# Kernel optimization log

Measured on AMD Instinct MI355X. Metric: run time of the kernel, lower is better.

Reference implementation:

```python
import jax, jax.numpy as jnp
import numpy as np

H = 48; W = 48; C_IN = 32; C_OUT = 64
L = 4                      # liftsamples
RADIUS = 3                 # neighborhood radius
CMCO = 16                  # LieConv PointConv fixed mid channels
FOCAL = W / np.pi          # equidistant fisheye focal
CX, CY = (W - 1) / 2.0, (H - 1) / 2.0
EPS = 1e-7


def _build_neighbor_indices(h, w, radius):
    offs = [(dx, dy) for dy in range(-radius, radius + 1)
            for dx in range(-radius, radius + 1)
            if dx * dx + dy * dy <= radius * radius]
    offs = np.array(offs, dtype=np.int64)  # (k,2) as (dx,dy)
    yy, xx = np.meshgrid(np.arange(h), np.arange(w), indexing='ij')
    yy = yy.reshape(-1, 1); xx = xx.reshape(-1, 1)
    ny = yy + offs[None, :, 1]; nx = xx + offs[None, :, 0]
    valid = (ny >= 0) & (ny < h) & (nx >= 0) & (nx < w)
    idx = ny * w + nx
    return np.where(valid, idx, -1).astype(np.int32)  # (h*w, k)


def swish(x):
    return x * jax.nn.sigmoid(x)


def so3_exp(wvec):
    # Rodrigues: (...,3) -> (...,3,3)
    th = jnp.maximum(jnp.linalg.norm(wvec, axis=-1, keepdims=True), EPS)
    k = wvec / th
    kx, ky, kz = k[..., 0], k[..., 1], k[..., 2]
    z = jnp.zeros_like(kx)
    K = jnp.stack([jnp.stack([z, -kz, ky], -1),
                   jnp.stack([kz, z, -kx], -1),
                   jnp.stack([-ky, kx, z], -1)], -2)
    th = th[..., None]
    I = jnp.eye(3, dtype=wvec.dtype)
    return I + jnp.sin(th) * K + (1.0 - jnp.cos(th)) * (K @ K)


def so3_log(R):
    # (...,3,3) -> (...,3)
    tr = R[..., 0, 0] + R[..., 1, 1] + R[..., 2, 2]
    cos = jnp.clip((tr - 1.0) * 0.5, -1.0 + 1e-6, 1.0 - 1e-6)
    th = jnp.arccos(cos)
    v = jnp.stack([R[..., 2, 1] - R[..., 1, 2],
                   R[..., 0, 2] - R[..., 2, 0],
                   R[..., 1, 0] - R[..., 0, 1]], -1)
    return v * (th / (2.0 * jnp.sin(th)))[..., None]


def setup_inputs() -> dict:
    key = jax.random.key(0)
    ks = jax.random.split(key, 6)
    def lin(k, fi, fo):
        return jax.random.normal(k, (fi, fo), jnp.float32) / np.sqrt(fi)
    return {
        'x': jax.random.normal(ks[0], (2, C_IN, H, W), jnp.float32),
        'neighbor_idx': jnp.asarray(_build_neighbor_indices(H, W, RADIUS)),
        'W1': lin(ks[1], 3, 32), 'b1': jnp.zeros((32,), jnp.float32),
        'W2': lin(ks[2], 32, 32), 'b2': jnp.zeros((32,), jnp.float32),
        'W3': lin(ks[3], 32, CMCO), 'b3': jnp.zeros((CMCO,), jnp.float32),
        'Wl': lin(ks[4], CMCO * C_IN, C_OUT), 'bl': jnp.zeros((C_OUT,), jnp.float32),
    }


def _lift_log(dtype):
    # pixel grid -> unit rays -> so(3) log of lifted group elems, shape (n*L, 3)
    u = jnp.arange(W, dtype=dtype); v = jnp.arange(H, dtype=dtype)
    uu, vv = jnp.meshgrid(u, v)               # 'xy' indexing, (H,W)
    dx = (uu - CX).reshape(-1); dy = (vv - CY).reshape(-1)
    r = jnp.sqrt(dx * dx + dy * dy)
    theta = r / FOCAL
    rs = jnp.maximum(r, EPS)
    rays = jnp.stack([jnp.sin(theta) * dx / rs,
                      jnp.sin(theta) * dy / rs,
                      jnp.cos(theta)], -1)    # (n,3)
    pz = jnp.clip(rays[:, 2], -1.0 + 1e-6, 1.0 - 1e-6)
    ang = jnp.arccos(pz)
    axis = jnp.stack([-rays[:, 1], rays[:, 0], jnp.zeros_like(pz)], -1)
    axis = axis / jnp.maximum(jnp.linalg.norm(axis, axis=-1, keepdims=True), EPS)
    Rp = so3_exp(axis * ang[:, None])          # (n,3,3), Rp @ e3 = ray
    alphas = jnp.arange(L, dtype=dtype) * (2.0 * np.pi / L)
    Rz = so3_exp(jnp.stack([jnp.zeros_like(alphas), jnp.zeros_like(alphas), alphas], -1))
    Rlift = jnp.einsum('nij,ljk->nlik', Rp, Rz)  # (n,L,3,3)
    return so3_log(Rlift).reshape(H * W * L, 3)


def reference(x, neighbor_idx, W1, b1, W2, b2, W3, b3, Wl, bl):
    bs, c, h, w = x.shape
    n = h * w
    k = neighbor_idx.shape[1]
    nL, K = n * L, k * L

    a = _lift_log(x.dtype)                                   # (nL,3)

    valid = neighbor_idx >= 0                                # (n,k)
    safe_pix = jnp.maximum(neighbor_idx, 0).astype(jnp.int32)
    # lifted neighbor indices: query lift copy l sees all (j, l') neighbors
    nb_lift = safe_pix[:, None, :, None] * L + jnp.arange(L, dtype=jnp.int32)[None, None, None, :]
    nb_lift = jnp.broadcast_to(nb_lift, (n, L, k, L)).reshape(nL, K)
    nb_pix = jnp.broadcast_to(safe_pix[:, None, :, None], (n, L, k, L)).reshape(nL, K)
    mask = jnp.broadcast_to(valid[:, None, :, None], (n, L, k, L)).reshape(nL, K)

    # pairwise group elements: log(exp(-b) @ exp(a))
    b_log = a[nb_lift]                                       # (nL,K,3)
    Rab = jnp.einsum('qmij,qjk->qmik', so3_exp(-b_log), so3_exp(a))
    ab = so3_log(Rab)                                        # (nL,K,3)

    # kernel MLP (WeightNet: 3 -> 32 -> 32 -> 16, swish)
    hdn = swish(ab @ W1 + b1)
    hdn = swish(hdn @ W2 + b2)
    wts = swish(hdn @ W3 + b3)                               # (nL,K,16)
    wts = jnp.where(mask[..., None], wts, 0.0)

    values = x.transpose(0, 2, 3, 1).reshape(bs, n, c)       # (bs,n,c)
    nv = values[:, nb_pix]                                   # (bs,nL,K,c)
    partial = jnp.einsum('bqmc,qmf->bqcf', nv, wts).reshape(bs, nL, c * CMCO)
    out = partial @ Wl + bl                                  # (bs,nL,c_out)
    out = out.reshape(bs, n, L, -1).mean(axis=2)             # pool over lift samples
    return out.reshape(bs, h, w, -1).transpose(0, 3, 1, 2)   # (bs,c_out,h,w)
```

## Files before the change

### kernel.cpp

```cpp
#include <hip/hip_runtime.h>

#define WW   48
#define NPIX 2304
#define CIN  32
#define COUT 64
#define KNB  29
#define FCO  16
#define NPJ  (NPIX * KNB)
#define GEN_WAVES  ((NPJ + 6) / 7)
#define GEN_BLOCKS ((GEN_WAVES + 3) / 4)
#define EDGE_BLOCKS ((NPIX * 6 + 1 + 255) / 256)

#define WS_RP64 0
#define WS_EG   165888
#define WS_M0   1050624
#define WS_V    1050688
#define WS_PART 4257856

__device__ __forceinline__ float swish_f(float x) {
    return x * __builtin_amdgcn_rcpf(1.0f + __expf(-x));
}

__device__ __forceinline__ void so3_exp_d(double wx, double wy, double wz, double R[9]) {
    double n  = sqrt(wx * wx + wy * wy + wz * wz);
    double th = fmax(n, 1e-7);
    double kx = wx / th, ky = wy / th, kz = wz / th;
    double s = sin(th), c = cos(th);
    double omc = 1.0 - c;
    R[0] = 1.0 + omc * (kx * kx - 1.0);
    R[1] = -s * kz + omc * kx * ky;
    R[2] =  s * ky + omc * kx * kz;
    R[3] =  s * kz + omc * kx * ky;
    R[4] = 1.0 + omc * (ky * ky - 1.0);
    R[5] = -s * kx + omc * ky * kz;
    R[6] = -s * ky + omc * kz * kx;
    R[7] =  s * kx + omc * kz * ky;
    R[8] = 1.0 + omc * (kz * kz - 1.0);
}

__device__ __forceinline__ void compute_Rp_d(int p, double R[9]) {
    int ui = p % WW, vi = p / WW;
    double dx = (double)ui - 23.5;
    double dy = (double)vi - 23.5;
    double r  = sqrt(dx * dx + dy * dy);
    const double FOCAL = 48.0 / 3.14159265358979323846;
    double theta = r / FOCAL;
    double rs = fmax(r, 1e-7);
    double st = sin(theta);
    double rayx = st * dx / rs;
    double rayy = st * dy / rs;
    double rayz = cos(theta);
    double pz  = fmin(fmax(rayz, -1.0 + 1e-6), 1.0 - 1e-6);
    double ang = acos(pz);
    double ax = -rayy, ay = rayx;
    double an = fmax(sqrt(ax * ax + ay * ay), 1e-7);
    ax /= an; ay /= an;
    so3_exp_d(ax * ang, ay * ang, 0.0, R);
}

__device__ __forceinline__ void mlp_half(float ab0, float ab1, float ab2, const int Q0,
    const float* __restrict__ W1, const float* __restrict__ b1,
    const float* __restrict__ W2, const float* __restrict__ b2,
    const float* __restrict__ W3, const float* __restrict__ b3,
    float* acc3) {
    float accq[16];
    #pragma unroll
    for (int q = 0; q < 16; ++q) accq[q] = b2[Q0 + q];
    #pragma unroll
    for (int i = 0; i < 32; ++i) {
        float h = swish_f(b1[i] + ab0 * W1[i] + ab1 * W1[32 + i] + ab2 * W1[64 + i]);
        #pragma unroll
        for (int q = 0; q < 16; ++q) accq[q] += h * W2[i * 32 + Q0 + q];
    }
    #pragma unroll
    for (int q = 0; q < 16; ++q) {
        float h2 = swish_f(accq[q]);
        #pragma unroll
        for (int f = 0; f < FCO; ++f) acc3[f] += h2 * W3[(Q0 + q) * FCO + f];
    }
}

__device__ __forceinline__ void mlp_eval(float ab0, float ab1, float ab2,
    const float* __restrict__ W1, const float* __restrict__ b1,
    const float* __restrict__ W2, const float* __restrict__ b2,
    const float* __restrict__ W3, const float* __restrict__ b3,
    float* o) {
    float acc3[FCO];
    #pragma unroll
    for (int f = 0; f < FCO; ++f) acc3[f] = b3[f];
    mlp_half(ab0, ab1, ab2, 0,  W1, b1, W2, b2, W3, b3, acc3);
    __builtin_amdgcn_sched_barrier(0);
    mlp_half(ab0, ab1, ab2, 16, W1, b1, W2, b2, W3, b3, acc3);
    #pragma unroll
    for (int f = 0; f < FCO; ++f) o[f] = swish_f(acc3[f]);
}

__global__ __launch_bounds__(256)
void rp_kernel(double* __restrict__ rp64) {
    int p = blockIdx.x * 256 + threadIdx.x;
    if (p >= NPIX) return;
    double R[9];
    compute_Rp_d(p, R);
    #pragma unroll
    for (int e = 0; e < 9; ++e) rp64[p * 9 + e] = R[e];
}

__global__ __launch_bounds__(256)
void vlog2_kernel(const int* __restrict__ nbr, const double* __restrict__ rp64,
                  float* __restrict__ vws) {
    int tid = blockIdx.x * 256 + threadIdx.x;
    if (tid >= NPJ * 4) return;
    int g2 = tid >> 2;
    int d  = tid & 3;
    int p = g2 / KNB, j = g2 - p * KNB;
    int pj = max(nbr[p * KNB + j], 0);
    double Rq[9];
    #pragma unroll
    for (int q = 0; q < 9; ++q) Rq[q] = rp64[p * 9 + q];
    double X[9];
    #pragma unroll
    for (int q = 0; q < 9; ++q) X[q] = 0.0;
    #pragma unroll
    for (int k = 0; k < 3; ++k) {
        double rn0 = rp64[pj * 9 + k * 3 + 0];
        double rn1 = rp64[pj * 9 + k * 3 + 1];
        double rn2 = rp64[pj * 9 + k * 3 + 2];
        #pragma unroll
        for (int jj = 0; jj < 3; ++jj) {
            X[0 * 3 + jj] += rn0 * Rq[k * 3 + jj];
            X[1 * 3 + jj] += rn1 * Rq[k * 3 + jj];
            X[2 * 3 + jj] += rn2 * Rq[k * 3 + jj];
        }
    }
    double c = (d == 0) ? 1.0 : ((d == 2) ? -1.0 : 0.0);
    double s = (d == 1) ? 1.0 : ((d == 3) ? -1.0 : 0.0);
    double M0 =  X[0] * c + X[1] * s;
    double M1 = -X[0] * s + X[1] * c;
    double M2 =  X[2];
    double M3 =  X[3] * c + X[4] * s;
    double M4 = -X[3] * s + X[4] * c;
    double M5 =  X[5];
    double M6 =  X[6] * c + X[7] * s;
    double M7 = -X[6] * s + X[7] * c;
    double M8 =  X[8];
    double tr   = M0 + M4 + M8;
    double cosv = fmin(fmax((tr - 1.0) * 0.5, -1.0 + 1e-6), 1.0 - 1e-6);
    double th   = acos(cosv);
    double svv  = sqrt((1.0 - cosv) * (1.0 + cosv));
    double fac  = th / (2.0 * svv);
    float* dst = vws + g2 * 12 + d * 3;
    dst[0] = (float)((M7 - M5) * fac);
    dst[1] = (float)((M2 - M6) * fac);
    dst[2] = (float)((M3 - M1) * fac);
}

__global__ __launch_bounds__(256)
void mlp1_kernel(const int* __restrict__ nbr,
                 const float* __restrict__ W1, const float* __restrict__ b1,
                 const float* __restrict__ W2, const float* __restrict__ b2,
                 const float* __restrict__ W3, const float* __restrict__ b3,
                 const double* __restrict__ rp64, const float* __restrict__ vws,
                 float* __restrict__ eg, float* __restrict__ m0v,
                 float* __restrict__ part) {
    if (blockIdx.x < GEN_BLOCKS) {
        int wave = blockIdx.x * 4 + (threadIdx.x >> 6);
        int lane = threadIdx.x & 63;
        int slot = lane / 9;
        int e    = lane - slot * 9;
        int g2   = wave * 7 + slot;
        int g2c  = min(g2, NPJ - 1);
        int l1m = e / 3, l2m = e - l1m * 3;
        int l1 = l1m + (l1m >> 1);
        int l2 = l2m + (l2m >> 1);
        int d  = (l1 - l2) & 3;
        const float* vp = vws + g2c * 12 + d * 3;
        float v0 = vp[0], v1 = vp[1], v2 = vp[2];
        float ab0 = (l2m == 0) ? v0 : ((l2m == 1) ?  v1 : -v1);
        float ab1 = (l2m == 0) ? v1 : ((l2m == 1) ? -v0 :  v0);
        float o[FCO];
        mlp_eval(ab0, ab1, v2, W1, b1, W2, b2, W3, b3, o);
        #pragma unroll
        for (int f = 0; f < FCO; ++f) {
            float a = o[f];
            a += __shfl(a, min(lane + 1, 63)) + __shfl(a, min(lane + 2, 63));
            a += __shfl(a, min(lane + 3, 63)) + __shfl(a, min(lane + 6, 63));
            o[f] = a;
        }
        if (e == 0 && lane < 63 && g2 < NPJ) {
            float* dst = part + g2 * FCO;
            #pragma unroll
            for (int f = 0; f < FCO; ++f) dst[f] = o[f];
        }
    } else {
        int g = (blockIdx.x - GEN_BLOCKS) * 256 + threadIdx.x;
        if (g > NPIX * 6) return;
        if (g == NPIX * 6) {
            float o[FCO];
            mlp_eval(0.f, 0.f, 0.f, W1, b1, W2, b2, W3, b3, o);
            #pragma unroll
            for (int f = 0; f < FCO; ++f) m0v[f] = o[f];
            return;
        }
        int pix = g / 6, which = g - pix * 6;
        double R[9];
        #pragma unroll
        for (int q = 0; q < 9; ++q) R[q] = rp64[pix * 9 + q];
        int m = (which < 3) ? which : (which - 3);
        int l = m + (m >> 1);
        double c = (l == 0) ? 1.0 : 0.0;
        double s = (l == 1) ? 1.0 : ((l == 3) ? -1.0 : 0.0);
        double M[9];
        #pragma unroll
        for (int i = 0; i < 3; ++i) {
            M[i * 3 + 0] =  R[i * 3 + 0] * c + R[i * 3 + 1] * s;
            M[i * 3 + 1] = -R[i * 3 + 0] * s + R[i * 3 + 1] * c;
            M[i * 3 + 2] =  R[i * 3 + 2];
        }
        double tr   = M[0] + M[4] + M[8];
        double cosv = fmin(fmax((tr - 1.0) * 0.5, -1.0 + 1e-6), 1.0 - 1e-6);
        double th   = acos(cosv);
        double sv   = sqrt((1.0 - cosv) * (1.0 + cosv));
        double fac  = th / (2.0 * sv);
        float sg = (which < 3) ? 1.f : -1.f;
        float o[FCO];
        mlp_eval(sg * (float)((M[7] - M[5]) * fac),
                 sg * (float)((M[2] - M[6]) * fac),
                 sg * (float)((M[3] - M[1]) * fac),
                 W1, b1, W2, b2, W3, b3, o);
        #pragma unroll
        for (int f = 0; f < FCO; ++f) eg[g * FCO + f] = o[f];
    }
}

__global__ __launch_bounds__(256)
void agg_kernel(const float* __restrict__ x, const int* __restrict__ nbr,
                const float* __restrict__ Wl, const float* __restrict__ bl,
                const float* __restrict__ eg, const float* __restrict__ m0v,
                const float* __restrict__ part, float* __restrict__ out) {
    __shared__ int   spj[KNB];
    __shared__ int   sval[KNB];
    __shared__ float sE[FCO];
    __shared__ float sS[KNB][FCO];
    __shared__ float sxv[2][CIN][KNB];
    __shared__ float sT[2][CIN][FCO];
    __shared__ float spp[256];

    const int p = blockIdx.x;
    const int t = threadIdx.x;

    if (t < KNB) {
        int idx = nbr[p * KNB + t];
        spj[t]  = max(idx, 0);
        sval[t] = (idx >= 0) ? 1 : 0;
    } else if (t >= 32 && t < 32 + FCO) {
        int f = t - 32;
        sE[f] = eg[(p * 6 + 0) * FCO + f] + eg[(p * 6 + 1) * FCO + f]
              + eg[(p * 6 + 2) * FCO + f] + m0v[f];
    }
    __syncthreads();

    for (int e = t; e < 2 * CIN * KNB; e += 256) {
        int bb = e / (CIN * KNB);
        int r  = e - bb * (CIN * KNB);
        int c  = r / KNB;
        int j  = r - c * KNB;
        sxv[bb][c][j] = x[bb * (CIN * NPIX) + c * NPIX + spj[j]];
    }
    for (int idx = t; idx < KNB * FCO; idx += 256) {
        int j = idx >> 4, f = idx & 15;
        float acc = part[(p * KNB + j) * FCO + f];
        int n6 = spj[j] * 6;
        acc += eg[(n6 + 3) * FCO + f] + eg[(n6 + 4) * FCO + f] + eg[(n6 + 5) * FCO + f];
        acc += sE[f];
        sS[j][f] = sval[j] ? acc * 0.25f : 0.f;
    }
    __syncthreads();

    for (int tt = t; tt < 2 * CIN * FCO; tt += 256) {
        int bb = tt >> 9;
        int c  = (tt >> 4) & 31;
        int f  = tt & 15;
        float acc = 0.f;
        #pragma unroll
        for (int j = 0; j < KNB; ++j)
            acc += sxv[bb][c][j] * sS[j][f];
        sT[bb][c][f] = acc;
    }
    __syncthreads();

    {
        int half = t >> 7, q = t & 127, bb = q >> 6, co = q & 63;
        const float* Tb = &sT[bb][0][0];
        float acc = 0.f;
        int cf0 = half * 256;
        #pragma unroll 8
        for (int cf = cf0; cf < cf0 + 256; ++cf)
            acc += Tb[cf] * Wl[cf * COUT + co];
        spp[t] = acc;
    }
    __syncthreads();
    if (t < 128) {
        int bb = t >> 6, co = t & 63;
        out[bb * (COUT * NPIX) + co * NPIX + p] = spp[t] + spp[t + 128] + bl[co];
    }
}

extern "C" void kernel_launch(void* const* d_in, const int* in_sizes, int n_in,
                              void* d_out, int out_size, void* d_ws, size_t ws_size,
                              hipStream_t stream) {
    const float* x  = (const float*)d_in[0];
    const int* nbr  = (const int*)d_in[1];
    const float* W1 = (const float*)d_in[2];
    const float* b1 = (const float*)d_in[3];
    const float* W2 = (const float*)d_in[4];
    const float* b2 = (const float*)d_in[5];
    const float* W3 = (const float*)d_in[6];
    const float* b3 = (const float*)d_in[7];
    const float* Wl = (const float*)d_in[8];
    const float* bl = (const float*)d_in[9];
    float* out = (float*)d_out;

    char* ws = (char*)d_ws;
    double* rp64 = (double*)(ws + WS_RP64);
    float*  eg   = (float*)(ws + WS_EG);
    float*  m0v  = (float*)(ws + WS_M0);
    float*  vws  = (float*)(ws + WS_V);
    float*  part = (float*)(ws + WS_PART);

    hipLaunchKernelGGL(rp_kernel, dim3((NPIX + 255) / 256), dim3(256), 0, stream,
                       rp64);
    hipLaunchKernelGGL(vlog2_kernel, dim3((NPJ * 4 + 255) / 256), dim3(256), 0, stream,
                       nbr, rp64, vws);
    hipLaunchKernelGGL(mlp1_kernel, dim3(GEN_BLOCKS + EDGE_BLOCKS), dim3(256), 0, stream,
                       nbr, W1, b1, W2, b2, W3, b3, rp64, vws, eg, m0v, part);
    hipLaunchKernelGGL(agg_kernel, dim3(NPIX), dim3(256), 0, stream,
                       x, nbr, Wl, bl, eg, m0v, part, out);
}
```

Baseline: 86.80 us.

## Move per-pixel edge MLP into rotation kernel and share Wl loads across batches

The per-pixel edge MLP evaluations (6 per pixel plus the zero-argument one) move out of the mlp1 kernel into the first kernel, which now runs 7 threads per pixel. Each thread recomputes the pixel rotation instead of reading it back from workspace. The mlp1 kernel now handles only the pairwise neighbor MLP. Separately, the final Wl projection in agg_kernel uses 128 threads that each serve both batch items from one Wl load, instead of 256 threads each loading Wl for one batch item. This halves Wl traffic but leaves half the block idle during that phase.

```diff
diff --git a/kernel.cpp b/kernel.cpp
--- a/kernel.cpp
+++ b/kernel.cpp
@@ -9,7 +9,6 @@
 #define NPJ  (NPIX * KNB)
 #define GEN_WAVES  ((NPJ + 6) / 7)
 #define GEN_BLOCKS ((GEN_WAVES + 3) / 4)
-#define EDGE_BLOCKS ((NPIX * 6 + 1 + 255) / 256)
 
 #define WS_RP64 0
 #define WS_EG   165888
@@ -96,13 +95,51 @@
 }
 
 __global__ __launch_bounds__(256)
-void rp_kernel(double* __restrict__ rp64) {
-    int p = blockIdx.x * 256 + threadIdx.x;
-    if (p >= NPIX) return;
+void rpe_kernel(const float* __restrict__ W1, const float* __restrict__ b1,
+                const float* __restrict__ W2, const float* __restrict__ b2,
+                const float* __restrict__ W3, const float* __restrict__ b3,
+                double* __restrict__ rp64, float* __restrict__ eg,
+                float* __restrict__ m0v) {
+    int tid = blockIdx.x * 256 + threadIdx.x;
+    if (tid >= NPIX * 7) return;
+    int p = tid / 7, which = tid - p * 7;
     double R[9];
     compute_Rp_d(p, R);
-    #pragma unroll
-    for (int e = 0; e < 9; ++e) rp64[p * 9 + e] = R[e];
+    if (which == 0) {
+        #pragma unroll
+        for (int e = 0; e < 9; ++e) rp64[p * 9 + e] = R[e];
+    }
+    int w = (which == 0) ? 0 : (which - 1);
+    int m = (w < 3) ? w : (w - 3);
+    float sg = (which == 0) ? 0.f : ((w < 3) ? 1.f : -1.f);
+    int l = m + (m >> 1);
+    double c = (l == 0) ? 1.0 : 0.0;
+    double s = (l == 1) ? 1.0 : ((l == 3) ? -1.0 : 0.0);
+    double M[9];
+    #pragma unroll
+    for (int i = 0; i < 3; ++i) {
+        M[i * 3 + 0] =  R[i * 3 + 0] * c + R[i * 3 + 1] * s;
+        M[i * 3 + 1] = -R[i * 3 + 0] * s + R[i * 3 + 1] * c;
+        M[i * 3 + 2] =  R[i * 3 + 2];
+    }
+    double tr   = M[0] + M[4] + M[8];
+    double cosv = fmin(fmax((tr - 1.0) * 0.5, -1.0 + 1e-6), 1.0 - 1e-6);
+    double th   = acos(cosv);
+    double sv   = sqrt((1.0 - cosv) * (1.0 + cosv));
+    double fac  = th / (2.0 * sv);
+    float o[FCO];
+    mlp_eval(sg * (float)((M[7] - M[5]) * fac),
+             sg * (float)((M[2] - M[6]) * fac),
+             sg * (float)((M[3] - M[1]) * fac),
+             W1, b1, W2, b2, W3, b3, o);
+    if (which > 0) {
+        float* dst = eg + (p * 6 + w) * FCO;
+        #pragma unroll
+        for (int f = 0; f < FCO; ++f) dst[f] = o[f];
+    } else if (p == 0) {
+        #pragma unroll
+        for (int f = 0; f < FCO; ++f) m0v[f] = o[f];
+    }
 }
 
 __global__ __launch_bounds__(256)
@@ -155,80 +192,37 @@
 }
 
 __global__ __launch_bounds__(256)
-void mlp1_kernel(const int* __restrict__ nbr,
-                 const float* __restrict__ W1, const float* __restrict__ b1,
+void mlp1_kernel(const float* __restrict__ W1, const float* __restrict__ b1,
                  const float* __restrict__ W2, const float* __restrict__ b2,
                  const float* __restrict__ W3, const float* __restrict__ b3,
-                 const double* __restrict__ rp64, const float* __restrict__ vws,
-                 float* __restrict__ eg, float* __restrict__ m0v,
-                 float* __restrict__ part) {
-    if (blockIdx.x < GEN_BLOCKS) {
-        int wave = blockIdx.x * 4 + (threadIdx.x >> 6);
-        int lane = threadIdx.x & 63;
-        int slot = lane / 9;
-        int e    = lane - slot * 9;
-        int g2   = wave * 7 + slot;
-        int g2c  = min(g2, NPJ - 1);
-        int l1m = e / 3, l2m = e - l1m * 3;
-        int l1 = l1m + (l1m >> 1);
-        int l2 = l2m + (l2m >> 1);
-        int d  = (l1 - l2) & 3;
-        const float* vp = vws + g2c * 12 + d * 3;
-        float v0 = vp[0], v1 = vp[1], v2 = vp[2];
-        float ab0 = (l2m == 0) ? v0 : ((l2m == 1) ?  v1 : -v1);
-        float ab1 = (l2m == 0) ? v1 : ((l2m == 1) ? -v0 :  v0);
-        float o[FCO];
-        mlp_eval(ab0, ab1, v2, W1, b1, W2, b2, W3, b3, o);
-        #pragma unroll
-        for (int f = 0; f < FCO; ++f) {
-            float a = o[f];
-            a += __shfl(a, min(lane + 1, 63)) + __shfl(a, min(lane + 2, 63));
-            a += __shfl(a, min(lane + 3, 63)) + __shfl(a, min(lane + 6, 63));
-            o[f] = a;
-        }
-        if (e == 0 && lane < 63 && g2 < NPJ) {
-            float* dst = part + g2 * FCO;
-            #pragma unroll
-            for (int f = 0; f < FCO; ++f) dst[f] = o[f];
-        }
-    } else {
-        int g = (blockIdx.x - GEN_BLOCKS) * 256 + threadIdx.x;
-        if (g > NPIX * 6) return;
-        if (g == NPIX * 6) {
-            float o[FCO];
-            mlp_eval(0.f, 0.f, 0.f, W1, b1, W2, b2, W3, b3, o);
-            #pragma unroll
-            for (int f = 0; f < FCO; ++f) m0v[f] = o[f];
-            return;
-        }
-        int pix = g / 6, which = g - pix * 6;
-        double R[9];
-        #pragma unroll
-        for (int q = 0; q < 9; ++q) R[q] = rp64[pix * 9 + q];
-        int m = (which < 3) ? which : (which - 3);
-        int l = m + (m >> 1);
-        double c = (l == 0) ? 1.0 : 0.0;
-        double s = (l == 1) ? 1.0 : ((l == 3) ? -1.0 : 0.0);
-        double M[9];
-        #pragma unroll
-        for (int i = 0; i < 3; ++i) {
-            M[i * 3 + 0] =  R[i * 3 + 0] * c + R[i * 3 + 1] * s;
-            M[i * 3 + 1] = -R[i * 3 + 0] * s + R[i * 3 + 1] * c;
-            M[i * 3 + 2] =  R[i * 3 + 2];
-        }
-        double tr   = M[0] + M[4] + M[8];
-        double cosv = fmin(fmax((tr - 1.0) * 0.5, -1.0 + 1e-6), 1.0 - 1e-6);
-        double th   = acos(cosv);
-        double sv   = sqrt((1.0 - cosv) * (1.0 + cosv));
-        double fac  = th / (2.0 * sv);
-        float sg = (which < 3) ? 1.f : -1.f;
-        float o[FCO];
-        mlp_eval(sg * (float)((M[7] - M[5]) * fac),
-                 sg * (float)((M[2] - M[6]) * fac),
-                 sg * (float)((M[3] - M[1]) * fac),
-                 W1, b1, W2, b2, W3, b3, o);
-        #pragma unroll
-        for (int f = 0; f < FCO; ++f) eg[g * FCO + f] = o[f];
+                 const float* __restrict__ vws, float* __restrict__ part) {
+    int wave = blockIdx.x * 4 + (threadIdx.x >> 6);
+    int lane = threadIdx.x & 63;
+    int slot = lane / 9;
+    int e    = lane - slot * 9;
+    int g2   = wave * 7 + slot;
+    int g2c  = min(g2, NPJ - 1);
+    int l1m = e / 3, l2m = e - l1m * 3;
+    int l1 = l1m + (l1m >> 1);
+    int l2 = l2m + (l2m >> 1);
+    int d  = (l1 - l2) & 3;
+    const float* vp = vws + g2c * 12 + d * 3;
+    float v0 = vp[0], v1 = vp[1], v2 = vp[2];
+    float ab0 = (l2m == 0) ? v0 : ((l2m == 1) ?  v1 : -v1);
+    float ab1 = (l2m == 0) ? v1 : ((l2m == 1) ? -v0 :  v0);
+    float o[FCO];
+    mlp_eval(ab0, ab1, v2, W1, b1, W2, b2, W3, b3, o);
+    #pragma unroll
+    for (int f = 0; f < FCO; ++f) {
+        float a = o[f];
+        a += __shfl(a, min(lane + 1, 63)) + __shfl(a, min(lane + 2, 63));
+        a += __shfl(a, min(lane + 3, 63)) + __shfl(a, min(lane + 6, 63));
+        o[f] = a;
+    }
+    if (e == 0 && lane < 63 && g2 < NPJ) {
+        float* dst = part + g2 * FCO;
+        #pragma unroll
+        for (int f = 0; f < FCO; ++f) dst[f] = o[f];
     }
 }
 
@@ -288,20 +282,26 @@
     }
     __syncthreads();
 
-    {
-        int half = t >> 7, q = t & 127, bb = q >> 6, co = q & 63;
-        const float* Tb = &sT[bb][0][0];
-        float acc = 0.f;
+    if (t < 128) {
+        int half = t >> 6, co = t & 63;
+        const float* Tb0 = &sT[0][0][0];
+        const float* Tb1 = &sT[1][0][0];
+        float a0 = 0.f, a1 = 0.f;
         int cf0 = half * 256;
         #pragma unroll 8
-        for (int cf = cf0; cf < cf0 + 256; ++cf)
-            acc += Tb[cf] * Wl[cf * COUT + co];
-        spp[t] = acc;
+        for (int cf = cf0; cf < cf0 + 256; ++cf) {
+            float w = Wl[cf * COUT + co];
+            a0 += Tb0[cf] * w;
+            a1 += Tb1[cf] * w;
+        }
+        spp[half * 128 + 0 * 64 + co] = a0;
+        spp[half * 128 + 1 * 64 + co] = a1;
     }
     __syncthreads();
     if (t < 128) {
         int bb = t >> 6, co = t & 63;
-        out[bb * (COUT * NPIX) + co * NPIX + p] = spp[t] + spp[t + 128] + bl[co];
+        out[bb * (COUT * NPIX) + co * NPIX + p] =
+            spp[0 * 128 + bb * 64 + co] + spp[1 * 128 + bb * 64 + co] + bl[co];
     }
 }
 
@@ -327,12 +327,12 @@
     float*  vws  = (float*)(ws + WS_V);
     float*  part = (float*)(ws + WS_PART);
 
-    hipLaunchKernelGGL(rp_kernel, dim3((NPIX + 255) / 256), dim3(256), 0, stream,
-                       rp64);
+    hipLaunchKernelGGL(rpe_kernel, dim3((NPIX * 7 + 255) / 256), dim3(256), 0, stream,
+                       W1, b1, W2, b2, W3, b3, rp64, eg, m0v);
     hipLaunchKernelGGL(vlog2_kernel, dim3((NPJ * 4 + 255) / 256), dim3(256), 0, stream,
                        nbr, rp64, vws);
-    hipLaunchKernelGGL(mlp1_kernel, dim3(GEN_BLOCKS + EDGE_BLOCKS), dim3(256), 0, stream,
-                       nbr, W1, b1, W2, b2, W3, b3, rp64, vws, eg, m0v, part);
+    hipLaunchKernelGGL(mlp1_kernel, dim3(GEN_BLOCKS), dim3(256), 0, stream,
+                       W1, b1, W2, b2, W3, b3, vws, part);
     hipLaunchKernelGGL(agg_kernel, dim3(NPIX), dim3(256), 0, stream,
                        x, nbr, Wl, bl, eg, m0v, part, out);
 }
```

Result: slower. 94.00 us (+8.3%).
